# Kernel optimization log

Measured on AMD Instinct MI355X. Metric: run time of the kernel, lower is better.

Reference implementation:

```python
import jax, jax.numpy as jnp
import numpy as np

B, T, D, H = 4, 2048, 1024, 16


def setup_inputs() -> dict:
    key = jax.random.key(0)
    ks = jax.random.split(key, 5)
    s = 0.02  # keep activations sane
    return {
        "x": jax.random.normal(ks[0], (B, T, D), jnp.float32),
        "Wq": jax.random.normal(ks[1], (D, D), jnp.float32) * s,
        "bq": jnp.zeros((D,), jnp.float32),
        "Wk": jax.random.normal(ks[2], (D, D), jnp.float32) * s,
        "bk": jnp.zeros((D,), jnp.float32),
        "Wv": jax.random.normal(ks[3], (D, D), jnp.float32) * s,
        "bv": jnp.zeros((D,), jnp.float32),
        "Wo": jax.random.normal(ks[4], (D, D), jnp.float32) * s,
        "bo": jnp.zeros((D,), jnp.float32),
    }


def _split_heads(t):  # (B,T,D) -> (B,H,T,d)
    b, s, d = t.shape
    return t.reshape(b, s, H, d // H).transpose(0, 2, 1, 3)


def reference(x, Wq, bq, Wk, bk, Wv, bv, Wo, bo):
    d_k = D // H
    q = _split_heads(x @ Wq + bq)  # (B,H,T,d)
    k = _split_heads(x @ Wk + bk)
    v = _split_heads(x @ Wv + bv)
    # scaled dot-product similarities (B,H,T,T)
    scores = jnp.einsum("bhqd,bhkd->bhqk", q, k) / jnp.sqrt(jnp.asarray(d_k, x.dtype))
    # causal mask: masked_fill(tril==0, -inf)
    causal = jnp.tril(jnp.ones((T, T), bool))
    scores = jnp.where(causal, scores, -jnp.inf)
    attn = jax.nn.softmax(scores, axis=-1)
    ctx = jnp.einsum("bhqk,bhkd->bhqd", attn, v)  # (B,H,T,d)
    ctx = ctx.transpose(0, 2, 1, 3).reshape(x.shape[0], T, D)
    return ctx @ Wo + bo
```

## Files before the change

kernel.cpp:

```cpp
#include <hip/hip_runtime.h>
#include <hip/hip_bf16.h>

typedef unsigned short u16;
typedef __attribute__((ext_vector_type(8))) short bf16x8;
typedef __attribute__((ext_vector_type(4))) short bf16x4;
typedef __attribute__((ext_vector_type(4))) float f32x4;

#define DD 1024
#define TT 2048
#define HH 16
#define BB 4
#define DK 64
#define MM 8192

#define QSCALE 0.180336880f

__device__ __forceinline__ u16 f2b(float x) {
  __hip_bfloat16 h = __float2bfloat16(x);
  return *reinterpret_cast<u16*>(&h);
}

#define GLD16(gp, lp)                                                         \
  __builtin_amdgcn_global_load_lds(                                           \
      (const __attribute__((address_space(1))) unsigned int*)(gp),            \
      (__attribute__((address_space(3))) unsigned int*)(lp), 16, 0, 0)

__global__ __launch_bounds__(256) void cast_bf16_kernel(
    const float* __restrict__ src, u16* __restrict__ dst, int n) {
  int i = (blockIdx.x * 256 + threadIdx.x) * 4;
  if (i + 3 < n) {
    float4 v = *reinterpret_cast<const float4*>(src + i);
    ushort4 o;
    o.x = f2b(v.x); o.y = f2b(v.y); o.z = f2b(v.z); o.w = f2b(v.w);
    *reinterpret_cast<ushort4*>(dst + i) = o;
  }
}

__global__ __launch_bounds__(256) void transpose_cast_kernel(
    const float* __restrict__ W0, const float* __restrict__ W1,
    const float* __restrict__ W2, const float* __restrict__ W3,
    u16* __restrict__ O0, u16* __restrict__ O1,
    u16* __restrict__ O2, u16* __restrict__ O3) {
  const float* W; u16* O;
  switch (blockIdx.z) {
    case 0: W = W0; O = O0; break;
    case 1: W = W1; O = O1; break;
    case 2: W = W2; O = O2; break;
    default: W = W3; O = O3; break;
  }
  __shared__ float tile[32][33];
  int tx = threadIdx.x, ty = threadIdx.y;
  int bx = blockIdx.x * 32;
  int by = blockIdx.y * 32;
#pragma unroll
  for (int j = 0; j < 4; j++)
    tile[ty + j * 8][tx] = W[(size_t)(by + ty + j * 8) * DD + bx + tx];
  __syncthreads();
#pragma unroll
  for (int j = 0; j < 4; j++)
    O[(size_t)(bx + ty + j * 8) * DD + by + tx] = f2b(tile[tx][ty + j * 8]);
}

__global__ __launch_bounds__(256) void gemm_qkv_kernel(
    const u16* __restrict__ A,
    const u16* __restrict__ WtQ, const u16* __restrict__ WtK,
    const u16* __restrict__ WtV,
    const float* __restrict__ bq, const float* __restrict__ bk,
    const float* __restrict__ bv,
    u16* __restrict__ Qo, u16* __restrict__ Ko, u16* __restrict__ Vo) {
  __shared__ __align__(16) u16 As[128 * 32];
  __shared__ __align__(16) u16 Bs[128 * 32];
  __shared__ __align__(16) u16 Vs[128 * 136];
  int z = blockIdx.z;
  const u16* Bt = (z == 0) ? WtQ : ((z == 1) ? WtK : WtV);
  const float* bias = (z == 0) ? bq : ((z == 1) ? bk : bv);
  int tid = threadIdx.x;
  int wave = tid >> 6, lane = tid & 63;
  int quad = lane >> 4, l16 = lane & 15;
  int m0 = blockIdx.x * 128, n0 = blockIdx.y * 128;
  int wm = (wave >> 1) * 64, wn = (wave & 1) * 64;

  f32x4 acc[4][4];
#pragma unroll
  for (int i = 0; i < 4; i++)
#pragma unroll
    for (int j = 0; j < 4; j++) acc[i][j] = (f32x4){0.f, 0.f, 0.f, 0.f};

  for (int k0 = 0; k0 < DD; k0 += 32) {
#pragma unroll
    for (int c = 0; c < 2; c++) {
      int idx = tid * 8 + c * 2048;
      int row = idx >> 5, kk = idx & 31;
      GLD16(A + (size_t)(m0 + row) * DD + k0 + kk, As + idx);
      GLD16(Bt + (size_t)(n0 + row) * DD + k0 + kk, Bs + idx);
    }
    __syncthreads();
    bf16x8 af[4], bfr[4];
#pragma unroll
    for (int mb = 0; mb < 4; mb++)
      af[mb] = *reinterpret_cast<const bf16x8*>(&As[(wm + mb * 16 + l16) * 32 + quad * 8]);
#pragma unroll
    for (int nb = 0; nb < 4; nb++)
      bfr[nb] = *reinterpret_cast<const bf16x8*>(&Bs[(wn + nb * 16 + l16) * 32 + quad * 8]);
#pragma unroll
    for (int mb = 0; mb < 4; mb++)
#pragma unroll
      for (int nb = 0; nb < 4; nb++)
        acc[mb][nb] = __builtin_amdgcn_mfma_f32_16x16x32_bf16(
            af[mb], bfr[nb], acc[mb][nb], 0, 0, 0);
    __syncthreads();
  }

  if (z == 2) {
#pragma unroll
    for (int mb = 0; mb < 4; mb++)
#pragma unroll
      for (int nb = 0; nb < 4; nb++) {
        int col = wn + nb * 16 + l16;
        float bv2 = bias[n0 + col];
#pragma unroll
        for (int r = 0; r < 4; r++) {
          int row = wm + mb * 16 + quad * 4 + r;
          Vs[col * 136 + row] = f2b(acc[mb][nb][r] + bv2);
        }
      }
    __syncthreads();
    int b = m0 >> 11;
    int tloc = m0 & 2047;
#pragma unroll
    for (int i = 0; i < 8; i++) {
      int idx = tid * 8 + i * 2048;
      int row = idx >> 7, col = idx & 127;
      uint4 v = *reinterpret_cast<const uint4*>(&Vs[row * 136 + col]);
      int ncol = n0 + row, h = ncol >> 6, dd = ncol & 63;
      *reinterpret_cast<uint4*>(
          Vo + (((size_t)(b * HH + h) * DK) + dd) * TT + tloc + col) = v;
    }
    return;
  }

  u16* outp = (z == 0) ? Qo : Ko;
  float scale = (z == 0) ? QSCALE : 1.0f;
#pragma unroll
  for (int mb = 0; mb < 4; mb++) {
#pragma unroll
    for (int nb = 0; nb < 4; nb++) {
      int col = n0 + wn + nb * 16 + l16;
      float bv2 = bias[col];
#pragma unroll
      for (int r = 0; r < 4; r++) {
        int row = m0 + wm + mb * 16 + quad * 4 + r;
        float val = (acc[mb][nb][r] + bv2) * scale;
        int hh = col >> 6, dd = col & 63;
        int b = row >> 11, t = row & 2047;
        outp[(((size_t)(b * HH + hh) * TT) + t) * DK + dd] = f2b(val);
      }
    }
  }
}

__global__ __launch_bounds__(256) void gemm_out_kernel(
    const u16* __restrict__ A, const u16* __restrict__ Bt,
    const float* __restrict__ bias, float* __restrict__ outp) {
  __shared__ __align__(16) u16 As[128 * 32];
  __shared__ __align__(16) u16 Bs[128 * 32];
  int tid = threadIdx.x;
  int wave = tid >> 6, lane = tid & 63;
  int quad = lane >> 4, l16 = lane & 15;
  int m0 = blockIdx.x * 128, n0 = blockIdx.y * 128;
  int wm = (wave >> 1) * 64, wn = (wave & 1) * 64;

  f32x4 acc[4][4];
#pragma unroll
  for (int i = 0; i < 4; i++)
#pragma unroll
    for (int j = 0; j < 4; j++) acc[i][j] = (f32x4){0.f, 0.f, 0.f, 0.f};

  for (int k0 = 0; k0 < DD; k0 += 32) {
#pragma unroll
    for (int c = 0; c < 2; c++) {
      int idx = tid * 8 + c * 2048;
      int row = idx >> 5, kk = idx & 31;
      GLD16(A + (size_t)(m0 + row) * DD + k0 + kk, As + idx);
      GLD16(Bt + (size_t)(n0 + row) * DD + k0 + kk, Bs + idx);
    }
    __syncthreads();
    bf16x8 af[4], bfr[4];
#pragma unroll
    for (int mb = 0; mb < 4; mb++)
      af[mb] = *reinterpret_cast<const bf16x8*>(&As[(wm + mb * 16 + l16) * 32 + quad * 8]);
#pragma unroll
    for (int nb = 0; nb < 4; nb++)
      bfr[nb] = *reinterpret_cast<const bf16x8*>(&Bs[(wn + nb * 16 + l16) * 32 + quad * 8]);
#pragma unroll
    for (int mb = 0; mb < 4; mb++)
#pragma unroll
      for (int nb = 0; nb < 4; nb++)
        acc[mb][nb] = __builtin_amdgcn_mfma_f32_16x16x32_bf16(
            af[mb], bfr[nb], acc[mb][nb], 0, 0, 0);
    __syncthreads();
  }

#pragma unroll
  for (int mb = 0; mb < 4; mb++) {
#pragma unroll
    for (int nb = 0; nb < 4; nb++) {
      int col = n0 + wn + nb * 16 + l16;
      float bv = bias[col];
#pragma unroll
      for (int r = 0; r < 4; r++) {
        int row = m0 + wm + mb * 16 + quad * 4 + r;
        outp[(size_t)row * DD + col] = acc[mb][nb][r] + bv;
      }
    }
  }
}

__global__ __launch_bounds__(512, 4) void attn_kernel(
    const u16* __restrict__ Q, const u16* __restrict__ K,
    const u16* __restrict__ VT, u16* __restrict__ ctx) {
  __shared__ __align__(16) u16 Ks[2][64][72];
  __shared__ __align__(16) u16 Vt[2][64][72];
  __shared__ float fbuf[8][16];

  int tid = threadIdx.x;
  int wave = tid >> 6, lane = tid & 63;
  int quad = lane >> 4, l16 = lane & 15;
  int bid = blockIdx.x;
  int bh = bid & 63;
  int px = bid >> 6;
  int b = bh >> 4, h = bh & 15;
  const u16* Qh = Q + (size_t)bh * TT * DK;
  const u16* Kh = K + (size_t)bh * TT * DK;
  const u16* Vh = VT + (size_t)bh * DK * TT;
  int sidx = tid * 8;

  for (int phase = 0; phase < 2; phase++) {
    int qt = phase ? (15 - px) : px;
    int ktmax = 2 * qt + 1;
    int dtile = 2 * qt + (wave >> 2);
    int qrl = (wave * 16 + l16) & 63;
    __syncthreads();

    const u16* qrow = Qh + (size_t)(qt * 128 + wave * 16 + l16) * DK + quad * 8;
    bf16x8 qf0 = *reinterpret_cast<const bf16x8*>(qrow);
    bf16x8 qf1 = *reinterpret_cast<const bf16x8*>(qrow + 32);

    uint4 kpre = *reinterpret_cast<const uint4*>(Kh + sidx);
    uint4 vpre = *reinterpret_cast<const uint4*>(Vh + (size_t)(sidx >> 6) * TT + (sidx & 63));
    *reinterpret_cast<uint4*>(&Ks[0][sidx >> 6][sidx & 63]) = kpre;
    *reinterpret_cast<uint4*>(&Vt[0][sidx >> 6][sidx & 63]) = vpre;
    __syncthreads();

    f32x4 oacc[4];
#pragma unroll
    for (int dt = 0; dt < 4; dt++) oacc[dt] = (f32x4){0.f, 0.f, 0.f, 0.f};
    float lsum = 0.f;

    for (int kt = 0; kt <= ktmax; kt++) {
      int cur = kt & 1, nxt = cur ^ 1;
      bool more = kt < ktmax;
      if (more) {
        kpre = *reinterpret_cast<const uint4*>(Kh + (size_t)(kt + 1) * 4096 + sidx);
        vpre = *reinterpret_cast<const uint4*>(
            Vh + (size_t)(sidx >> 6) * TT + (kt + 1) * 64 + (sidx & 63));
      }

      if (kt <= dtile) {
        f32x4 sacc[4];
#pragma unroll
        for (int kb = 0; kb < 4; kb++) sacc[kb] = (f32x4){0.f, 0.f, 0.f, 0.f};
#pragma unroll
        for (int kb = 0; kb < 4; kb++) {
          bf16x8 kf0 = *reinterpret_cast<const bf16x8*>(&Ks[cur][kb * 16 + l16][quad * 8]);
          bf16x8 kf1 = *reinterpret_cast<const bf16x8*>(&Ks[cur][kb * 16 + l16][32 + quad * 8]);
          sacc[kb] = __builtin_amdgcn_mfma_f32_16x16x32_bf16(kf0, qf0, sacc[kb], 0, 0, 0);
          sacc[kb] = __builtin_amdgcn_mfma_f32_16x16x32_bf16(kf1, qf1, sacc[kb], 0, 0, 0);
        }

        if (kt == dtile) {
#pragma unroll
          for (int kb = 0; kb < 4; kb++)
#pragma unroll
            for (int r = 0; r < 4; r++)
              if (kb * 16 + quad * 4 + r > qrl) sacc[kb][r] = -__builtin_inff();
        }

#pragma unroll
        for (int kb = 0; kb < 4; kb++) {
          float p0 = exp2f(sacc[kb][0]), p1 = exp2f(sacc[kb][1]);
          float p2 = exp2f(sacc[kb][2]), p3 = exp2f(sacc[kb][3]);
          lsum += (p0 + p1) + (p2 + p3);
          union { unsigned u[2]; bf16x4 v; } pk;
          pk.u[0] = (unsigned)f2b(p0) | ((unsigned)f2b(p1) << 16);
          pk.u[1] = (unsigned)f2b(p2) | ((unsigned)f2b(p3) << 16);
#pragma unroll
          for (int dt = 0; dt < 4; dt++) {
            bf16x4 vf = *reinterpret_cast<const bf16x4*>(
                &Vt[cur][dt * 16 + l16][kb * 16 + quad * 4]);
            oacc[dt] = __builtin_amdgcn_mfma_f32_16x16x16bf16_1k(pk.v, vf, oacc[dt], 0, 0, 0);
          }
        }
      }

      if (more) {
        *reinterpret_cast<uint4*>(&Ks[nxt][sidx >> 6][sidx & 63]) = kpre;
        *reinterpret_cast<uint4*>(&Vt[nxt][sidx >> 6][sidx & 63]) = vpre;
      }
      __syncthreads();
    }

    lsum += __shfl_xor(lsum, 16);
    lsum += __shfl_xor(lsum, 32);
    if (quad == 0) fbuf[wave][l16] = lsum;
    asm volatile("s_waitcnt lgkmcnt(0)" ::: "memory");
    f32x4 lv = *reinterpret_cast<const f32x4*>(&fbuf[wave][quad * 4]);
    f32x4 inv;
#pragma unroll
    for (int r = 0; r < 4; r++) inv[r] = 1.0f / lv[r];

    u16* Obuf = &Ks[0][0][0];
#pragma unroll
    for (int dt = 0; dt < 4; dt++)
#pragma unroll
      for (int r = 0; r < 4; r++)
        Obuf[(wave * 16 + quad * 4 + r) * 72 + dt * 16 + l16] =
            f2b(oacc[dt][r] * inv[r]);
    asm volatile("s_waitcnt lgkmcnt(0)" ::: "memory");
#pragma unroll
    for (int i = 0; i < 2; i++) {
      int idx = lane * 8 + i * 512;
      int row = idx >> 6, colc = idx & 63;
      uint4 v = *reinterpret_cast<const uint4*>(&Obuf[(wave * 16 + row) * 72 + colc]);
      int t = qt * 128 + wave * 16 + row;
      *reinterpret_cast<uint4*>(
          ctx + ((size_t)(b * TT + t)) * DD + h * DK + colc) = v;
    }
  }
}

extern "C" void kernel_launch(void* const* d_in, const int* in_sizes, int n_in,
                              void* d_out, int out_size, void* d_ws, size_t ws_size,
                              hipStream_t stream) {
  const float* x  = (const float*)d_in[0];
  const float* Wq = (const float*)d_in[1];
  const float* bq = (const float*)d_in[2];
  const float* Wk = (const float*)d_in[3];
  const float* bk = (const float*)d_in[4];
  const float* Wv = (const float*)d_in[5];
  const float* bv = (const float*)d_in[6];
  const float* Wo = (const float*)d_in[7];
  const float* bo = (const float*)d_in[8];
  float* out = (float*)d_out;

  char* ws = (char*)d_ws;
  size_t off = 0;
  u16* xb  = (u16*)(ws + off); off += (size_t)MM * DD * 2;
  u16* wtq = (u16*)(ws + off); off += (size_t)DD * DD * 2;
  u16* wtk = (u16*)(ws + off); off += (size_t)DD * DD * 2;
  u16* wtv = (u16*)(ws + off); off += (size_t)DD * DD * 2;
  u16* wto = (u16*)(ws + off); off += (size_t)DD * DD * 2;
  u16* Qb  = (u16*)(ws + off); off += (size_t)MM * DD * 2;
  u16* Kb  = (u16*)(ws + off); off += (size_t)MM * DD * 2;
  u16* VTb = (u16*)(ws + off); off += (size_t)MM * DD * 2;
  u16* ctx = (u16*)(ws + off); off += (size_t)MM * DD * 2;

  {
    int n = MM * DD;
    cast_bf16_kernel<<<n / 1024, 256, 0, stream>>>(x, xb, n);
  }
  {
    dim3 grid(DD / 32, DD / 32, 4);
    dim3 block(32, 8);
    transpose_cast_kernel<<<grid, block, 0, stream>>>(Wq, Wk, Wv, Wo, wtq, wtk, wtv, wto);
  }
  {
    dim3 grid(MM / 128, DD / 128, 3);
    gemm_qkv_kernel<<<grid, 256, 0, stream>>>(xb, wtq, wtk, wtv, bq, bk, bv,
                                              Qb, Kb, VTb);
  }
  {
    attn_kernel<<<512, 512, 0, stream>>>(Qb, Kb, VTb, ctx);
  }
  {
    dim3 grid(MM / 128, DD / 128);
    gemm_out_kernel<<<grid, 256, 0, stream>>>(ctx, wto, bo, out);
  }
}
```

Measured before the change: 273.2 us.

## Split attention blocks per query tile and compute row sums via MFMA

Result: slower. 339.9 us (+24.4%).

```diff
diff --git a/kernel.cpp b/kernel.cpp
--- a/kernel.cpp
+++ b/kernel.cpp
@@ -18,6 +18,14 @@
 __device__ __forceinline__ u16 f2b(float x) {
   __hip_bfloat16 h = __float2bfloat16(x);
   return *reinterpret_cast<u16*>(&h);
+}
+
+__device__ __forceinline__ unsigned pk2(float a, float b) {
+  float2 t; t.x = a; t.y = b;
+  __hip_bfloat162 h = __float22bfloat162_rn(t);
+  union { __hip_bfloat162 h; unsigned u; } cv;
+  cv.h = h;
+  return cv.u;
 }
 
 #define GLD16(gp, lp)                                                         \
@@ -216,126 +224,119 @@
   }
 }
 
-__global__ __launch_bounds__(512, 4) void attn_kernel(
+__global__ __launch_bounds__(512, 8) void attn_kernel(
     const u16* __restrict__ Q, const u16* __restrict__ K,
     const u16* __restrict__ VT, u16* __restrict__ ctx) {
   __shared__ __align__(16) u16 Ks[2][64][72];
   __shared__ __align__(16) u16 Vt[2][64][72];
-  __shared__ float fbuf[8][16];
 
   int tid = threadIdx.x;
   int wave = tid >> 6, lane = tid & 63;
   int quad = lane >> 4, l16 = lane & 15;
   int bid = blockIdx.x;
   int bh = bid & 63;
-  int px = bid >> 6;
+  int qt = 15 - (bid >> 6);
   int b = bh >> 4, h = bh & 15;
   const u16* Qh = Q + (size_t)bh * TT * DK;
   const u16* Kh = K + (size_t)bh * TT * DK;
   const u16* Vh = VT + (size_t)bh * DK * TT;
   int sidx = tid * 8;
 
-  for (int phase = 0; phase < 2; phase++) {
-    int qt = phase ? (15 - px) : px;
-    int ktmax = 2 * qt + 1;
-    int dtile = 2 * qt + (wave >> 2);
-    int qrl = (wave * 16 + l16) & 63;
-    __syncthreads();
-
-    const u16* qrow = Qh + (size_t)(qt * 128 + wave * 16 + l16) * DK + quad * 8;
-    bf16x8 qf0 = *reinterpret_cast<const bf16x8*>(qrow);
-    bf16x8 qf1 = *reinterpret_cast<const bf16x8*>(qrow + 32);
-
-    uint4 kpre = *reinterpret_cast<const uint4*>(Kh + sidx);
-    uint4 vpre = *reinterpret_cast<const uint4*>(Vh + (size_t)(sidx >> 6) * TT + (sidx & 63));
-    *reinterpret_cast<uint4*>(&Ks[0][sidx >> 6][sidx & 63]) = kpre;
-    *reinterpret_cast<uint4*>(&Vt[0][sidx >> 6][sidx & 63]) = vpre;
-    __syncthreads();
-
-    f32x4 oacc[4];
-#pragma unroll
-    for (int dt = 0; dt < 4; dt++) oacc[dt] = (f32x4){0.f, 0.f, 0.f, 0.f};
-    float lsum = 0.f;
-
-    for (int kt = 0; kt <= ktmax; kt++) {
-      int cur = kt & 1, nxt = cur ^ 1;
-      bool more = kt < ktmax;
-      if (more) {
-        kpre = *reinterpret_cast<const uint4*>(Kh + (size_t)(kt + 1) * 4096 + sidx);
-        vpre = *reinterpret_cast<const uint4*>(
-            Vh + (size_t)(sidx >> 6) * TT + (kt + 1) * 64 + (sidx & 63));
-      }
-
-      if (kt <= dtile) {
-        f32x4 sacc[4];
-#pragma unroll
-        for (int kb = 0; kb < 4; kb++) sacc[kb] = (f32x4){0.f, 0.f, 0.f, 0.f};
-#pragma unroll
-        for (int kb = 0; kb < 4; kb++) {
-          bf16x8 kf0 = *reinterpret_cast<const bf16x8*>(&Ks[cur][kb * 16 + l16][quad * 8]);
-          bf16x8 kf1 = *reinterpret_cast<const bf16x8*>(&Ks[cur][kb * 16 + l16][32 + quad * 8]);
-          sacc[kb] = __builtin_amdgcn_mfma_f32_16x16x32_bf16(kf0, qf0, sacc[kb], 0, 0, 0);
-          sacc[kb] = __builtin_amdgcn_mfma_f32_16x16x32_bf16(kf1, qf1, sacc[kb], 0, 0, 0);
+  int ktmax = 2 * qt + 1;
+  int dtile = 2 * qt + (wave >> 2);
+  int qrl = (wave * 16 + l16) & 63;
+
+  const u16* qrow = Qh + (size_t)(qt * 128 + wave * 16 + l16) * DK + quad * 8;
+  bf16x8 qf0 = *reinterpret_cast<const bf16x8*>(qrow);
+  bf16x8 qf1 = *reinterpret_cast<const bf16x8*>(qrow + 32);
+
+  uint4 kpre = *reinterpret_cast<const uint4*>(Kh + sidx);
+  uint4 vpre = *reinterpret_cast<const uint4*>(Vh + (size_t)(sidx >> 6) * TT + (sidx & 63));
+  *reinterpret_cast<uint4*>(&Ks[0][sidx >> 6][sidx & 63]) = kpre;
+  *reinterpret_cast<uint4*>(&Vt[0][sidx >> 6][sidx & 63]) = vpre;
+  __syncthreads();
+
+  f32x4 oacc[4];
+#pragma unroll
+  for (int dt = 0; dt < 4; dt++) oacc[dt] = (f32x4){0.f, 0.f, 0.f, 0.f};
+  f32x4 lacc = (f32x4){0.f, 0.f, 0.f, 0.f};
+  const bf16x4 ones = (bf16x4){0x3F80, 0x3F80, 0x3F80, 0x3F80};
+
+  for (int kt = 0; kt <= ktmax; kt++) {
+    int cur = kt & 1, nxt = cur ^ 1;
+    bool more = kt < ktmax;
+    if (more) {
+      kpre = *reinterpret_cast<const uint4*>(Kh + (size_t)(kt + 1) * 4096 + sidx);
+      vpre = *reinterpret_cast<const uint4*>(
+          Vh + (size_t)(sidx >> 6) * TT + (kt + 1) * 64 + (sidx & 63));
+    }
+
+    if (kt <= dtile) {
+      f32x4 sacc[4];
+#pragma unroll
+      for (int kb = 0; kb < 4; kb++) sacc[kb] = (f32x4){0.f, 0.f, 0.f, 0.f};
+#pragma unroll
+      for (int kb = 0; kb < 4; kb++) {
+        bf16x8 kf0 = *reinterpret_cast<const bf16x8*>(&Ks[cur][kb * 16 + l16][quad * 8]);
+        bf16x8 kf1 = *reinterpret_cast<const bf16x8*>(&Ks[cur][kb * 16 + l16][32 + quad * 8]);
+        sacc[kb] = __builtin_amdgcn_mfma_f32_16x16x32_bf16(kf0, qf0, sacc[kb], 0, 0, 0);
+        sacc[kb] = __builtin_amdgcn_mfma_f32_16x16x32_bf16(kf1, qf1, sacc[kb], 0, 0, 0);
+      }
+
+      if (kt == dtile) {
+#pragma unroll
+        for (int kb = 0; kb < 4; kb++)
+#pragma unroll
+          for (int r = 0; r < 4; r++)
+            if (kb * 16 + quad * 4 + r > qrl) sacc[kb][r] = -__builtin_inff();
+      }
+
+#pragma unroll
+      for (int kb = 0; kb < 4; kb++) {
+        float p0 = __builtin_amdgcn_exp2f(sacc[kb][0]);
+        float p1 = __builtin_amdgcn_exp2f(sacc[kb][1]);
+        float p2 = __builtin_amdgcn_exp2f(sacc[kb][2]);
+        float p3 = __builtin_amdgcn_exp2f(sacc[kb][3]);
+        union { unsigned u[2]; bf16x4 v; } pk;
+        pk.u[0] = pk2(p0, p1);
+        pk.u[1] = pk2(p2, p3);
+        lacc = __builtin_amdgcn_mfma_f32_16x16x16bf16_1k(pk.v, ones, lacc, 0, 0, 0);
+#pragma unroll
+        for (int dt = 0; dt < 4; dt++) {
+          bf16x4 vf = *reinterpret_cast<const bf16x4*>(
+              &Vt[cur][dt * 16 + l16][kb * 16 + quad * 4]);
+          oacc[dt] = __builtin_amdgcn_mfma_f32_16x16x16bf16_1k(pk.v, vf, oacc[dt], 0, 0, 0);
         }
-
-        if (kt == dtile) {
-#pragma unroll
-          for (int kb = 0; kb < 4; kb++)
-#pragma unroll
-            for (int r = 0; r < 4; r++)
-              if (kb * 16 + quad * 4 + r > qrl) sacc[kb][r] = -__builtin_inff();
-        }
-
-#pragma unroll
-        for (int kb = 0; kb < 4; kb++) {
-          float p0 = exp2f(sacc[kb][0]), p1 = exp2f(sacc[kb][1]);
-          float p2 = exp2f(sacc[kb][2]), p3 = exp2f(sacc[kb][3]);
-          lsum += (p0 + p1) + (p2 + p3);
-          union { unsigned u[2]; bf16x4 v; } pk;
-          pk.u[0] = (unsigned)f2b(p0) | ((unsigned)f2b(p1) << 16);
-          pk.u[1] = (unsigned)f2b(p2) | ((unsigned)f2b(p3) << 16);
-#pragma unroll
-          for (int dt = 0; dt < 4; dt++) {
-            bf16x4 vf = *reinterpret_cast<const bf16x4*>(
-                &Vt[cur][dt * 16 + l16][kb * 16 + quad * 4]);
-            oacc[dt] = __builtin_amdgcn_mfma_f32_16x16x16bf16_1k(pk.v, vf, oacc[dt], 0, 0, 0);
-          }
-        }
-      }
-
-      if (more) {
-        *reinterpret_cast<uint4*>(&Ks[nxt][sidx >> 6][sidx & 63]) = kpre;
-        *reinterpret_cast<uint4*>(&Vt[nxt][sidx >> 6][sidx & 63]) = vpre;
-      }
-      __syncthreads();
-    }
-
-    lsum += __shfl_xor(lsum, 16);
-    lsum += __shfl_xor(lsum, 32);
-    if (quad == 0) fbuf[wave][l16] = lsum;
-    asm volatile("s_waitcnt lgkmcnt(0)" ::: "memory");
-    f32x4 lv = *reinterpret_cast<const f32x4*>(&fbuf[wave][quad * 4]);
-    f32x4 inv;
-#pragma unroll
-    for (int r = 0; r < 4; r++) inv[r] = 1.0f / lv[r];
-
-    u16* Obuf = &Ks[0][0][0];
-#pragma unroll
-    for (int dt = 0; dt < 4; dt++)
-#pragma unroll
-      for (int r = 0; r < 4; r++)
-        Obuf[(wave * 16 + quad * 4 + r) * 72 + dt * 16 + l16] =
-            f2b(oacc[dt][r] * inv[r]);
-    asm volatile("s_waitcnt lgkmcnt(0)" ::: "memory");
-#pragma unroll
-    for (int i = 0; i < 2; i++) {
-      int idx = lane * 8 + i * 512;
-      int row = idx >> 6, colc = idx & 63;
-      uint4 v = *reinterpret_cast<const uint4*>(&Obuf[(wave * 16 + row) * 72 + colc]);
-      int t = qt * 128 + wave * 16 + row;
-      *reinterpret_cast<uint4*>(
-          ctx + ((size_t)(b * TT + t)) * DD + h * DK + colc) = v;
-    }
+      }
+    }
+
+    if (more) {
+      *reinterpret_cast<uint4*>(&Ks[nxt][sidx >> 6][sidx & 63]) = kpre;
+      *reinterpret_cast<uint4*>(&Vt[nxt][sidx >> 6][sidx & 63]) = vpre;
+    }
+    __syncthreads();
+  }
+
+  f32x4 inv;
+#pragma unroll
+  for (int r = 0; r < 4; r++) inv[r] = 1.0f / lacc[r];
+
+  u16* Obuf = &Ks[0][0][0];
+#pragma unroll
+  for (int dt = 0; dt < 4; dt++)
+#pragma unroll
+    for (int r = 0; r < 4; r++)
+      Obuf[(wave * 16 + quad * 4 + r) * 72 + dt * 16 + l16] =
+          f2b(oacc[dt][r] * inv[r]);
+  asm volatile("s_waitcnt lgkmcnt(0)" ::: "memory");
+#pragma unroll
+  for (int i = 0; i < 2; i++) {
+    int idx = lane * 8 + i * 512;
+    int row = idx >> 6, colc = idx & 63;
+    uint4 v = *reinterpret_cast<const uint4*>(&Obuf[(wave * 16 + row) * 72 + colc]);
+    int t = qt * 128 + wave * 16 + row;
+    *reinterpret_cast<uint4*>(
+        ctx + ((size_t)(b * TT + t)) * DD + h * DK + colc) = v;
   }
 }
 
@@ -380,7 +381,7 @@
                                               Qb, Kb, VTb);
   }
   {
-    attn_kernel<<<512, 512, 0, stream>>>(Qb, Kb, VTb, ctx);
+    attn_kernel<<<1024, 512, 0, stream>>>(Qb, Kb, VTb, ctx);
   }
   {
     dim3 grid(MM / 128, DD / 128);
```
